# Performance work log

Measured on AMD Instinct MI355X. Metric: run time of the kernel, lower is better.

The kernel has to match this reference:

```python
import jax, jax.numpy as jnp
import numpy as np

N_TOKEN = 64
H = 16
D = 1024
D_K = 64
D_V = 64
S3 = 30  # 3 * S, number of gated leading positions
GATE_INIT = 10.0


def setup_inputs() -> dict:
    key = jax.random.key(0)
    ks = jax.random.split(key, 8)
    B, L = 32, 2048
    x = jax.random.normal(ks[0], (B, L, D), dtype=jnp.float32)
    q_init = (1.0 / D_K) ** 0.5
    q_tok = jax.random.uniform(ks[1], (1, N_TOKEN, D), minval=-q_init, maxval=q_init, dtype=jnp.float32)
    scale = 0.02
    Wq = jax.random.normal(ks[2], (D, H * D_K), dtype=jnp.float32) * scale
    Wk = jax.random.normal(ks[3], (D, H * D_K), dtype=jnp.float32) * scale
    Wv = jax.random.normal(ks[4], (D, H * D_V), dtype=jnp.float32) * scale
    Wfc = jax.random.normal(ks[5], (H * D_V, D), dtype=jnp.float32) * scale
    gate_logit = -jnp.ones((S3,), dtype=jnp.float32) * GATE_INIT  # matches module init
    gamma = jnp.ones((D,), dtype=jnp.float32)
    beta = jnp.zeros((D,), dtype=jnp.float32)
    return {"x": x, "q_tok": q_tok, "Wq": Wq, "Wk": Wk, "Wv": Wv, "Wfc": Wfc,
            "gate_logit": gate_logit, "gamma": gamma, "beta": beta}


def reference(x, q_tok, Wq, Wk, Wv, Wfc, gate_logit, gamma, beta):
    # x: [B, L, D]; q_tok: [1, n_token, D]. Dropout is identity (eval mode).
    B, L, _ = x.shape
    temp = D_K ** 0.5

    # Cumulative-product gate over the first 30 positions (the torch for-loop).
    gate = jnp.cumprod(1.0 - jax.nn.sigmoid(gate_logit))  # [30]
    x1 = x.at[:, :S3].multiply(gate[None, :, None])

    q = (q_tok @ Wq).reshape(N_TOKEN, H, D_K)          # [n, H, dk]
    k = (x @ Wk).reshape(B, L, H, D_K)                  # [B, L, H, dk]
    v = (x1 @ Wv).reshape(B, L, H, D_V)                 # [B, L, H, dv]

    scores = jnp.einsum('nhd,blhd->bhnl', q / temp, k)  # [B, H, n, L]
    attn = jax.nn.softmax(scores, axis=-1)
    out = jnp.einsum('bhnl,blhd->bnhd', attn, v).reshape(B, N_TOKEN, H * D_V)

    out = out @ Wfc + q_tok                              # residual with query tokens

    # LayerNorm over last dim, eps=1e-6
    mu = jnp.mean(out, axis=-1, keepdims=True)
    var = jnp.mean(jnp.square(out - mu), axis=-1, keepdims=True)
    out = (out - mu) * jax.lax.rsqrt(var + 1e-6) * gamma + beta
    return out
```

## Files before the change

kernel.cpp:

```cpp
#include <hip/hip_runtime.h>
#include <stdint.h>

typedef unsigned short u16;
typedef short bf16x8 __attribute__((ext_vector_type(8)));
typedef float f32x4 __attribute__((ext_vector_type(4)));

__device__ __forceinline__ u16 f2b(float f) {
  uint32_t u = __builtin_bit_cast(uint32_t, f);
  u += 0x7fffu + ((u >> 16) & 1u);
  return (u16)(u >> 16);
}

__device__ __forceinline__ void gload_lds16(const void* g, void* l) {
  __builtin_amdgcn_global_load_lds(
      (const __attribute__((address_space(1))) void*)g,
      (__attribute__((address_space(3))) void*)l, 16, 0, 0);
}

__global__ __launch_bounds__(256) void cvt_kernel(const float* __restrict__ src,
                                                  u16* __restrict__ dst, int n8) {
  int stride = gridDim.x * 256;
  for (int idx = blockIdx.x * 256 + threadIdx.x; idx < n8; idx += stride) {
    int64_t i = (int64_t)idx * 8;
    float4 a = *(const float4*)(src + i);
    float4 b = *(const float4*)(src + i + 4);
    union { u16 u[8]; bf16x8 v; } o;
    o.u[0] = f2b(a.x); o.u[1] = f2b(a.y); o.u[2] = f2b(a.z); o.u[3] = f2b(a.w);
    o.u[4] = f2b(b.x); o.u[5] = f2b(b.y); o.u[6] = f2b(b.z); o.u[7] = f2b(b.w);
    *(bf16x8*)(dst + i) = o.v;
  }
}

__global__ __launch_bounds__(256) void transpose_all_kernel(
    const float* __restrict__ Wk, const float* __restrict__ Wv,
    const float* __restrict__ Wfc, const float* __restrict__ Wq,
    u16* __restrict__ wkvT, u16* __restrict__ wfcT, u16* __restrict__ wqT,
    const float* __restrict__ gl, float* __restrict__ gate) {
  if (blockIdx.x == 0 && threadIdx.x == 0) {
    float g = 1.0f;
    for (int i = 0; i < 30; ++i) {
      float s = 1.0f / (1.0f + __expf(-gl[i]));
      g *= (1.0f - s);
      gate[i] = g;
    }
  }
  __shared__ float ls[64][65];
  int which = blockIdx.x >> 8;
  int tile = blockIdx.x & 255;
  const float* src = (which == 0) ? Wk : (which == 1) ? Wv : (which == 2) ? Wfc : Wq;
  u16* dst = (which == 0) ? wkvT : (which == 1) ? (wkvT + 1024 * 1024)
           : (which == 2) ? wfcT : wqT;
  int t = threadIdx.x;
  int bx = tile & 15;
  int by = tile >> 4;
  int r0 = by * 64, c0 = bx * 64;
  int tr = t >> 6, tc = t & 63;
#pragma unroll
  for (int i = 0; i < 16; ++i)
    ls[tr + i * 4][tc] = src[(int64_t)(r0 + tr + i * 4) * 1024 + c0 + tc];
  __syncthreads();
#pragma unroll
  for (int i = 0; i < 16; ++i)
    dst[(int64_t)(c0 + tr + i * 4) * 1024 + r0 + tc] = f2b(ls[tc][tr + i * 4]);
}

__global__ __launch_bounds__(256, 4) void q_gemm_kernel(
    const u16* __restrict__ qtokb, const u16* __restrict__ wqT, u16* __restrict__ qb) {
  __shared__ u16 As[4096];
  __shared__ u16 Bs[8192];
  int n0 = blockIdx.x * 128;
  int t = threadIdx.x, w = t >> 6, lane = t & 63;
  int wn = w * 32;
  f32x4 acc[2][4] = {};
  int l3 = lane >> 3;
  int colE = ((lane & 7) ^ l3) * 8;
  const u16* aS = qtokb + (int64_t)(w * 16 + l3) * 1024 + colE;
  const u16* bS = wqT + (int64_t)(n0 + w * 32 + l3) * 1024 + colE;
  u16* aD = As + w * 1024;
  u16* bD = Bs + w * 2048;
  int l15 = lane & 15, g16 = lane >> 4;
  for (int kt = 0; kt < 16; ++kt) {
    int ko = kt * 64;
    __syncthreads();
    gload_lds16(aS + ko, aD);
    gload_lds16(aS + ko + 8192, aD + 512);
#pragma unroll
    for (int g = 0; g < 4; ++g) gload_lds16(bS + ko + g * 8192, bD + g * 512);
    __syncthreads();
#pragma unroll
    for (int kk = 0; kk < 2; ++kk) {
      int sl = ((kk * 4 + g16) ^ (l15 & 7)) * 8;
      bf16x8 af[4], bf[2];
#pragma unroll
      for (int j = 0; j < 4; ++j) af[j] = *(const bf16x8*)(As + (j * 16 + l15) * 64 + sl);
#pragma unroll
      for (int i = 0; i < 2; ++i) bf[i] = *(const bf16x8*)(Bs + (wn + i * 16 + l15) * 64 + sl);
#pragma unroll
      for (int i = 0; i < 2; ++i)
#pragma unroll
        for (int j = 0; j < 4; ++j)
          acc[i][j] = __builtin_amdgcn_mfma_f32_16x16x32_bf16(bf[i], af[j], acc[i][j], 0, 0, 0);
    }
  }
  const float sc = 1.44269504f / 8.0f;
  int lr = g16 * 4;
#pragma unroll
  for (int i = 0; i < 2; ++i) {
    int colg = n0 + wn + i * 16 + lr;
#pragma unroll
    for (int j = 0; j < 4; ++j) {
      int qrow = j * 16 + l15;
      u16 p[4];
#pragma unroll
      for (int r = 0; r < 4; ++r) p[r] = f2b(acc[i][j][r] * sc);
      *(uint64_t*)(qb + qrow * 1024 + colg) = *(uint64_t*)p;
    }
  }
}

__global__ __launch_bounds__(256, 2) void kv_gemm_kernel(
    const float* __restrict__ x, const u16* __restrict__ wkvT,
    const float* __restrict__ gate, u16* __restrict__ kbuf, u16* __restrict__ vT) {
  __shared__ u16 As[8192];
  __shared__ u16 Bs[8192];
  int d = blockIdx.x;
  int xc = d & 7;
  int nb = (d >> 3) & 15;
  int mb = (d >> 7) * 8 + xc;
  int m0 = mb * 128, n0 = nb * 128;
  int t = threadIdx.x, w = t >> 6, lane = t & 63;
  int wm = (w >> 1) * 64, wn = (w & 1) * 64;
  bool isV = (n0 >= 1024);
  f32x4 acc[4][4] = {};
  int l3 = lane >> 3;
  int colE = ((lane & 7) ^ l3) * 8;
  const float* aF = x + (int64_t)(m0 + w * 32 + l3) * 1024 + colE;
  const u16* bS = wkvT + (int64_t)(n0 + w * 32 + l3) * 1024 + colE;
  u16* aD = As + w * 2048;
  u16* bD = Bs + w * 2048;
  int l15 = lane & 15, g16 = lane >> 4;
  float4 r0a, r0b, r1a, r1b, r2a, r2b, r3a, r3b;
  r0a = *(const float4*)(aF);             r0b = *(const float4*)(aF + 4);
  r1a = *(const float4*)(aF + 8192);      r1b = *(const float4*)(aF + 8192 + 4);
  r2a = *(const float4*)(aF + 16384);     r2b = *(const float4*)(aF + 16384 + 4);
  r3a = *(const float4*)(aF + 24576);     r3b = *(const float4*)(aF + 24576 + 4);
  for (int kt = 0; kt < 16; ++kt) {
    int ko = kt * 64;
    __syncthreads();
    {
      u16 p[8];
#define CVT_WRITE(g, va, vb)                                                   \
      p[0] = f2b(va.x); p[1] = f2b(va.y); p[2] = f2b(va.z); p[3] = f2b(va.w);  \
      p[4] = f2b(vb.x); p[5] = f2b(vb.y); p[6] = f2b(vb.z); p[7] = f2b(vb.w);  \
      *(bf16x8*)((char*)(aD + (g) * 512) + lane * 16) = *(const bf16x8*)p;
      CVT_WRITE(0, r0a, r0b)
      CVT_WRITE(1, r1a, r1b)
      CVT_WRITE(2, r2a, r2b)
      CVT_WRITE(3, r3a, r3b)
#undef CVT_WRITE
    }
#pragma unroll
    for (int g = 0; g < 4; ++g)
      gload_lds16(bS + ko + g * 8192, bD + g * 512);
    __syncthreads();
    if (kt < 15) {
      int kn = ko + 64;
      r0a = *(const float4*)(aF + kn);          r0b = *(const float4*)(aF + kn + 4);
      r1a = *(const float4*)(aF + kn + 8192);   r1b = *(const float4*)(aF + kn + 8192 + 4);
      r2a = *(const float4*)(aF + kn + 16384);  r2b = *(const float4*)(aF + kn + 16384 + 4);
      r3a = *(const float4*)(aF + kn + 24576);  r3b = *(const float4*)(aF + kn + 24576 + 4);
    }
#pragma unroll
    for (int kk = 0; kk < 2; ++kk) {
      int sl = ((kk * 4 + g16) ^ (l15 & 7)) * 8;
      bf16x8 af[4], bf[4];
#pragma unroll
      for (int i = 0; i < 4; ++i) af[i] = *(const bf16x8*)(As + (wm + i * 16 + l15) * 64 + sl);
#pragma unroll
      for (int j = 0; j < 4; ++j) bf[j] = *(const bf16x8*)(Bs + (wn + j * 16 + l15) * 64 + sl);
      if (!isV) {
#pragma unroll
        for (int i = 0; i < 4; ++i)
#pragma unroll
          for (int j = 0; j < 4; ++j)
            acc[i][j] = __builtin_amdgcn_mfma_f32_16x16x32_bf16(bf[i], af[j], acc[i][j], 0, 0, 0);
      } else {
#pragma unroll
        for (int i = 0; i < 4; ++i)
#pragma unroll
          for (int j = 0; j < 4; ++j)
            acc[i][j] = __builtin_amdgcn_mfma_f32_16x16x32_bf16(af[i], bf[j], acc[i][j], 0, 0, 0);
      }
    }
  }
  int b = m0 >> 11, lbase = m0 & 2047;
  int lr = g16 * 4;
  if (!isV) {
#pragma unroll
    for (int i = 0; i < 4; ++i) {
      int dkg = n0 + wn + i * 16 + lr;
      int h = dkg >> 6, dkk = dkg & 63;
#pragma unroll
      for (int j = 0; j < 4; ++j) {
        int l = lbase + wm + j * 16 + l15;
        u16 p[4];
#pragma unroll
        for (int r = 0; r < 4; ++r) p[r] = f2b(acc[i][j][r]);
        *(uint64_t*)(kbuf + ((int64_t)((b * 16 + h) * 2048 + l)) * 64 + dkk) = *(uint64_t*)p;
      }
    }
  } else {
#pragma unroll
    for (int j = 0; j < 4; ++j) {
      int dvg = (n0 - 1024) + wn + j * 16 + l15;
      int h = dvg >> 6, dv = dvg & 63;
#pragma unroll
      for (int i = 0; i < 4; ++i) {
        int lg = lbase + wm + i * 16 + lr;
        u16 p[4];
#pragma unroll
        for (int r = 0; r < 4; ++r) {
          float val = acc[i][j][r];
          int ll = lg + r;
          if (ll < 30) val *= gate[ll];
          p[r] = f2b(val);
        }
        *(uint64_t*)(vT + ((int64_t)((b * 16 + h) * 64 + dv)) * 2048 + lg) = *(uint64_t*)p;
      }
    }
  }
}

__global__ __launch_bounds__(256) void attn_kernel(
    const u16* __restrict__ qb, const u16* __restrict__ kbuf,
    const u16* __restrict__ vT, float* __restrict__ pO,
    float* __restrict__ pm, float* __restrict__ ps) {
  __shared__ u16 Ps[4096];
  int bid = blockIdx.x;
  int b = bid >> 6, h = (bid >> 2) & 15, c = bid & 3;
  int t = threadIdx.x, w = t >> 6, lane = t & 63;
  int l15 = lane & 15, g16 = lane >> 4, lh8 = g16 * 8;
  bf16x8 qf0 = *(const bf16x8*)(qb + (w * 16 + l15) * 1024 + h * 64 + lh8);
  bf16x8 qf1 = *(const bf16x8*)(qb + (w * 16 + l15) * 1024 + h * 64 + 32 + lh8);
  const u16* kB = kbuf + (int64_t)(b * 16 + h) * (2048 * 64);
  const u16* vB = vT + (int64_t)(b * 16 + h) * (64 * 2048);
  char* PsW = (char*)Ps + w * 2048;
  float m_r[4] = {-1e30f, -1e30f, -1e30f, -1e30f};
  float s_r[4] = {0.f, 0.f, 0.f, 0.f};
  f32x4 O[4] = {};
  for (int lt = 0; lt < 8; ++lt) {
    int l0 = c * 512 + lt * 64;
    f32x4 S[4];
#pragma unroll
    for (int ls = 0; ls < 4; ++ls) {
      const u16* kr = kB + (l0 + ls * 16 + l15) * 64 + lh8;
      bf16x8 k0 = *(const bf16x8*)(kr);
      bf16x8 k1 = *(const bf16x8*)(kr + 32);
      f32x4 s = {};
      s = __builtin_amdgcn_mfma_f32_16x16x32_bf16(qf0, k0, s, 0, 0, 0);
      s = __builtin_amdgcn_mfma_f32_16x16x32_bf16(qf1, k1, s, 0, 0, 0);
      S[ls] = s;
    }
    float scale[4];
#pragma unroll
    for (int r = 0; r < 4; ++r) {
      float tm = fmaxf(fmaxf(S[0][r], S[1][r]), fmaxf(S[2][r], S[3][r]));
#pragma unroll
      for (int msk = 1; msk < 16; msk <<= 1)
        tm = fmaxf(tm, __shfl_xor(tm, msk, 16));
      float mn = fmaxf(m_r[r], tm);
      scale[r] = exp2f(m_r[r] - mn);
      m_r[r] = mn;
    }
#pragma unroll
    for (int ls = 0; ls < 4; ++ls)
#pragma unroll
      for (int r = 0; r < 4; ++r) S[ls][r] = exp2f(S[ls][r] - m_r[r]);
#pragma unroll
    for (int r = 0; r < 4; ++r) {
      float psm = (S[0][r] + S[1][r]) + (S[2][r] + S[3][r]);
      s_r[r] = s_r[r] * scale[r] + psm;
    }
#pragma unroll
    for (int ls = 0; ls < 4; ++ls)
#pragma unroll
      for (int r = 0; r < 4; ++r) {
        int row = g16 * 4 + r;
        int off = (ls * 16 + l15) * 2;
        *(u16*)(PsW + row * 128 + (off ^ ((row & 7) << 4))) = f2b(S[ls][r]);
      }
#pragma unroll
    for (int d = 0; d < 4; ++d)
#pragma unroll
      for (int r = 0; r < 4; ++r) O[d][r] *= scale[r];
    bf16x8 pa0, pa1;
    {
      int off0 = g16 * 16;
      pa0 = *(const bf16x8*)(PsW + l15 * 128 + (off0 ^ ((l15 & 7) << 4)));
      pa1 = *(const bf16x8*)(PsW + l15 * 128 + ((off0 + 64) ^ ((l15 & 7) << 4)));
    }
#pragma unroll
    for (int d = 0; d < 4; ++d) {
      const u16* vr = vB + (d * 16 + l15) * 2048 + l0 + lh8;
      bf16x8 v0 = *(const bf16x8*)(vr);
      bf16x8 v1 = *(const bf16x8*)(vr + 32);
      O[d] = __builtin_amdgcn_mfma_f32_16x16x32_bf16(pa0, v0, O[d], 0, 0, 0);
      O[d] = __builtin_amdgcn_mfma_f32_16x16x32_bf16(pa1, v1, O[d], 0, 0, 0);
    }
  }
#pragma unroll
  for (int r = 0; r < 4; ++r) {
    float s = s_r[r];
#pragma unroll
    for (int msk = 1; msk < 16; msk <<= 1) s += __shfl_xor(s, msk, 16);
    s_r[r] = s;
  }
  int64_t pbase = (int64_t)bid * 4096;
#pragma unroll
  for (int d = 0; d < 4; ++d)
#pragma unroll
    for (int r = 0; r < 4; ++r) {
      int n = w * 16 + g16 * 4 + r;
      pO[pbase + n * 64 + d * 16 + l15] = O[d][r];
    }
  if (l15 == 0) {
#pragma unroll
    for (int r = 0; r < 4; ++r) {
      int n = w * 16 + g16 * 4 + r;
      pm[bid * 64 + n] = m_r[r];
      ps[bid * 64 + n] = s_r[r];
    }
  }
}

__global__ __launch_bounds__(256) void attn_combine_kernel(
    const float* __restrict__ pO, const float* __restrict__ pm,
    const float* __restrict__ ps, u16* __restrict__ attnout) {
  int bh = blockIdx.x;
  int b = bh >> 4, h = bh & 15;
  int t = threadIdx.x;
  int dv = t & 63, grp = t >> 6;
#pragma unroll
  for (int i = 0; i < 16; ++i) {
    int n = grp * 16 + i;
    int base = bh * 256 + n;
    float m0 = pm[base], m1 = pm[base + 64], m2 = pm[base + 128], m3 = pm[base + 192];
    float M = fmaxf(fmaxf(m0, m1), fmaxf(m2, m3));
    float w0 = exp2f(m0 - M), w1 = exp2f(m1 - M), w2 = exp2f(m2 - M), w3 = exp2f(m3 - M);
    float stot = w0 * ps[base] + w1 * ps[base + 64] + w2 * ps[base + 128] + w3 * ps[base + 192];
    float inv = 1.0f / stot;
    int64_t ob = (int64_t)bh * 16384 + n * 64 + dv;
    float o = w0 * pO[ob] + w1 * pO[ob + 4096] + w2 * pO[ob + 8192] + w3 * pO[ob + 12288];
    attnout[((int64_t)(b * 64 + n)) * 1024 + h * 64 + dv] = f2b(o * inv);
  }
}

__global__ __launch_bounds__(256, 4) void fc_gemm_kernel(
    const u16* __restrict__ a, const u16* __restrict__ bT,
    const float* __restrict__ q_tok, float* __restrict__ out) {
  __shared__ u16 As[4096];
  __shared__ u16 Bs[8192];
  int m0 = (blockIdx.x >> 3) * 64;
  int n0 = (blockIdx.x & 7) * 128;
  int t = threadIdx.x, w = t >> 6, lane = t & 63;
  int wn = w * 32;
  f32x4 acc[2][4] = {};
  int l3 = lane >> 3;
  int colE = ((lane & 7) ^ l3) * 8;
  const u16* aS = a + (int64_t)(m0 + w * 16 + l3) * 1024 + colE;
  const u16* bS = bT + (int64_t)(n0 + w * 32 + l3) * 1024 + colE;
  u16* aD = As + w * 1024;
  u16* bD = Bs + w * 2048;
  int l15 = lane & 15, g16 = lane >> 4;
  for (int kt = 0; kt < 16; ++kt) {
    int ko = kt * 64;
    __syncthreads();
    gload_lds16(aS + ko, aD);
    gload_lds16(aS + ko + 8192, aD + 512);
#pragma unroll
    for (int g = 0; g < 4; ++g) gload_lds16(bS + ko + g * 8192, bD + g * 512);
    __syncthreads();
#pragma unroll
    for (int kk = 0; kk < 2; ++kk) {
      int sl = ((kk * 4 + g16) ^ (l15 & 7)) * 8;
      bf16x8 af[4], bf[2];
#pragma unroll
      for (int j = 0; j < 4; ++j) af[j] = *(const bf16x8*)(As + (j * 16 + l15) * 64 + sl);
#pragma unroll
      for (int i = 0; i < 2; ++i) bf[i] = *(const bf16x8*)(Bs + (wn + i * 16 + l15) * 64 + sl);
#pragma unroll
      for (int i = 0; i < 2; ++i)
#pragma unroll
        for (int j = 0; j < 4; ++j)
          acc[i][j] = __builtin_amdgcn_mfma_f32_16x16x32_bf16(bf[i], af[j], acc[i][j], 0, 0, 0);
    }
  }
  int lr = g16 * 4;
#pragma unroll
  for (int i = 0; i < 2; ++i) {
    int colg = n0 + wn + i * 16 + lr;
#pragma unroll
    for (int j = 0; j < 4; ++j) {
      int row = m0 + j * 16 + l15;
      float4 res = *(const float4*)(q_tok + (row & 63) * 1024 + colg);
      float4 o;
      o.x = acc[i][j][0] + res.x;
      o.y = acc[i][j][1] + res.y;
      o.z = acc[i][j][2] + res.z;
      o.w = acc[i][j][3] + res.w;
      *(float4*)(out + (int64_t)row * 1024 + colg) = o;
    }
  }
}

__global__ __launch_bounds__(256) void ln_kernel(
    const float* __restrict__ fc, const float* __restrict__ gamma,
    const float* __restrict__ beta, float* __restrict__ out) {
  __shared__ float red[8];
  int row = blockIdx.x, t = threadIdx.x;
  float4 y = *(const float4*)(fc + (int64_t)row * 1024 + t * 4);
  float s = (y.x + y.y) + (y.z + y.w);
  float ss = (y.x * y.x + y.y * y.y) + (y.z * y.z + y.w * y.w);
#pragma unroll
  for (int msk = 1; msk < 64; msk <<= 1) {
    s += __shfl_xor(s, msk, 64);
    ss += __shfl_xor(ss, msk, 64);
  }
  if ((t & 63) == 0) { red[t >> 6] = s; red[4 + (t >> 6)] = ss; }
  __syncthreads();
  s = (red[0] + red[1]) + (red[2] + red[3]);
  ss = (red[4] + red[5]) + (red[6] + red[7]);
  float mu = s * (1.0f / 1024.0f);
  float var = ss * (1.0f / 1024.0f) - mu * mu;
  float rstd = rsqrtf(var + 1e-6f);
  float4 g = *(const float4*)(gamma + t * 4);
  float4 be = *(const float4*)(beta + t * 4);
  float4 o;
  o.x = (y.x - mu) * rstd * g.x + be.x;
  o.y = (y.y - mu) * rstd * g.y + be.y;
  o.z = (y.z - mu) * rstd * g.z + be.z;
  o.w = (y.w - mu) * rstd * g.w + be.w;
  *(float4*)(out + (int64_t)row * 1024 + t * 4) = o;
}

extern "C" void kernel_launch(void* const* d_in, const int* in_sizes, int n_in,
                              void* d_out, int out_size, void* d_ws, size_t ws_size,
                              hipStream_t stream) {
  const float* x     = (const float*)d_in[0];
  const float* q_tok = (const float*)d_in[1];
  const float* Wq    = (const float*)d_in[2];
  const float* Wk    = (const float*)d_in[3];
  const float* Wv    = (const float*)d_in[4];
  const float* Wfc   = (const float*)d_in[5];
  const float* gl    = (const float*)d_in[6];
  const float* gamma = (const float*)d_in[7];
  const float* beta  = (const float*)d_in[8];
  float* out = (float*)d_out;
  char* ws = (char*)d_ws;

  u16*   kbuf    = (u16*)(ws + 134217728);
  u16*   vT      = (u16*)(ws + 268435456);
  u16*   wkvT    = (u16*)(ws + 402653184);
  u16*   wfcT    = (u16*)(ws + 406847488);
  u16*   wqT     = (u16*)(ws + 408944640);
  u16*   qtokb   = (u16*)(ws + 411041792);
  u16*   qb      = (u16*)(ws + 411172864);
  float* gate    = (float*)(ws + 411303936);
  u16*   attnout = (u16*)(ws + 411304448);
  float* fcout   = (float*)(ws + 415498752);
  float* pO = (float*)(ws);
  float* pm = (float*)(ws + 33554432);
  float* ps = (float*)(ws + 34078720);

  transpose_all_kernel<<<1024, 256, 0, stream>>>(Wk, Wv, Wfc, Wq, wkvT, wfcT, wqT, gl, gate);
  cvt_kernel<<<32, 256, 0, stream>>>(q_tok, qtokb, 8192);
  q_gemm_kernel<<<8, 256, 0, stream>>>(qtokb, wqT, qb);
  kv_gemm_kernel<<<8192, 256, 0, stream>>>(x, wkvT, gate, kbuf, vT);
  attn_kernel<<<2048, 256, 0, stream>>>(qb, kbuf, vT, pO, pm, ps);
  attn_combine_kernel<<<512, 256, 0, stream>>>(pO, pm, ps, attnout);
  fc_gemm_kernel<<<256, 256, 0, stream>>>(attnout, wfcT, q_tok, fcout);
  ln_kernel<<<2048, 256, 0, stream>>>(fcout, gamma, beta, out);
}
```

Measured before the change: 647.9 us.

## Remove split-L attention partials and fuse softmax normalization into attn kernel

The attention kernel now has each block walk the full sequence length for one (batch, head) pair instead of splitting it four ways. The separate combine kernel and its float partial-output, max and sum buffers are gone. Normalization and the bf16 store to the attention output happen directly in the attention kernel. This removes a launch and the partial-buffer traffic, but cuts the grid from 2048 to 512 blocks and quadruples the serial loop length. That lowers the parallelism available to hide memory latency on K/V reads.

```diff
diff --git a/kernel.cpp b/kernel.cpp
--- a/kernel.cpp
+++ b/kernel.cpp
@@ -233,11 +233,10 @@
 
 __global__ __launch_bounds__(256) void attn_kernel(
     const u16* __restrict__ qb, const u16* __restrict__ kbuf,
-    const u16* __restrict__ vT, float* __restrict__ pO,
-    float* __restrict__ pm, float* __restrict__ ps) {
-  __shared__ u16 Ps[4096];
+    const u16* __restrict__ vT, u16* __restrict__ attnout) {
+  __shared__ u16 Ps[8192];
   int bid = blockIdx.x;
-  int b = bid >> 6, h = (bid >> 2) & 15, c = bid & 3;
+  int b = bid >> 4, h = bid & 15;
   int t = threadIdx.x, w = t >> 6, lane = t & 63;
   int l15 = lane & 15, g16 = lane >> 4, lh8 = g16 * 8;
   bf16x8 qf0 = *(const bf16x8*)(qb + (w * 16 + l15) * 1024 + h * 64 + lh8);
@@ -248,8 +247,8 @@
   float m_r[4] = {-1e30f, -1e30f, -1e30f, -1e30f};
   float s_r[4] = {0.f, 0.f, 0.f, 0.f};
   f32x4 O[4] = {};
-  for (int lt = 0; lt < 8; ++lt) {
-    int l0 = c * 512 + lt * 64;
+  for (int lt = 0; lt < 32; ++lt) {
+    int l0 = lt * 64;
     f32x4 S[4];
 #pragma unroll
     for (int ls = 0; ls < 4; ++ls) {
@@ -313,46 +312,17 @@
     float s = s_r[r];
 #pragma unroll
     for (int msk = 1; msk < 16; msk <<= 1) s += __shfl_xor(s, msk, 16);
-    s_r[r] = s;
-  }
-  int64_t pbase = (int64_t)bid * 4096;
+    float inv = 1.0f / s;
+#pragma unroll
+    for (int d = 0; d < 4; ++d) O[d][r] *= inv;
+  }
 #pragma unroll
   for (int d = 0; d < 4; ++d)
 #pragma unroll
     for (int r = 0; r < 4; ++r) {
       int n = w * 16 + g16 * 4 + r;
-      pO[pbase + n * 64 + d * 16 + l15] = O[d][r];
-    }
-  if (l15 == 0) {
-#pragma unroll
-    for (int r = 0; r < 4; ++r) {
-      int n = w * 16 + g16 * 4 + r;
-      pm[bid * 64 + n] = m_r[r];
-      ps[bid * 64 + n] = s_r[r];
-    }
-  }
-}
-
-__global__ __launch_bounds__(256) void attn_combine_kernel(
-    const float* __restrict__ pO, const float* __restrict__ pm,
-    const float* __restrict__ ps, u16* __restrict__ attnout) {
-  int bh = blockIdx.x;
-  int b = bh >> 4, h = bh & 15;
-  int t = threadIdx.x;
-  int dv = t & 63, grp = t >> 6;
-#pragma unroll
-  for (int i = 0; i < 16; ++i) {
-    int n = grp * 16 + i;
-    int base = bh * 256 + n;
-    float m0 = pm[base], m1 = pm[base + 64], m2 = pm[base + 128], m3 = pm[base + 192];
-    float M = fmaxf(fmaxf(m0, m1), fmaxf(m2, m3));
-    float w0 = exp2f(m0 - M), w1 = exp2f(m1 - M), w2 = exp2f(m2 - M), w3 = exp2f(m3 - M);
-    float stot = w0 * ps[base] + w1 * ps[base + 64] + w2 * ps[base + 128] + w3 * ps[base + 192];
-    float inv = 1.0f / stot;
-    int64_t ob = (int64_t)bh * 16384 + n * 64 + dv;
-    float o = w0 * pO[ob] + w1 * pO[ob + 4096] + w2 * pO[ob + 8192] + w3 * pO[ob + 12288];
-    attnout[((int64_t)(b * 64 + n)) * 1024 + h * 64 + dv] = f2b(o * inv);
-  }
+      attnout[(int64_t)(b * 64 + n) * 1024 + h * 64 + d * 16 + l15] = f2b(O[d][r]);
+    }
 }
 
 __global__ __launch_bounds__(256, 4) void fc_gemm_kernel(
@@ -468,16 +438,12 @@
   float* gate    = (float*)(ws + 411303936);
   u16*   attnout = (u16*)(ws + 411304448);
   float* fcout   = (float*)(ws + 415498752);
-  float* pO = (float*)(ws);
-  float* pm = (float*)(ws + 33554432);
-  float* ps = (float*)(ws + 34078720);
 
   transpose_all_kernel<<<1024, 256, 0, stream>>>(Wk, Wv, Wfc, Wq, wkvT, wfcT, wqT, gl, gate);
   cvt_kernel<<<32, 256, 0, stream>>>(q_tok, qtokb, 8192);
   q_gemm_kernel<<<8, 256, 0, stream>>>(qtokb, wqT, qb);
   kv_gemm_kernel<<<8192, 256, 0, stream>>>(x, wkvT, gate, kbuf, vT);
-  attn_kernel<<<2048, 256, 0, stream>>>(qb, kbuf, vT, pO, pm, ps);
-  attn_combine_kernel<<<512, 256, 0, stream>>>(pO, pm, ps, attnout);
+  attn_kernel<<<512, 256, 0, stream>>>(qb, kbuf, vT, attnout);
   fc_gemm_kernel<<<256, 256, 0, stream>>>(attnout, wfcT, q_tok, fcout);
   ln_kernel<<<2048, 256, 0, stream>>>(fcout, gamma, beta, out);
 }
```

Result: slower. 680.0 us (+4.9%).
